# Kernel optimization log

Hardware: AMD Instinct MI355X
Metric: run time of the kernel (lower is better)

The kernel has to match this reference:

```python
import jax, jax.numpy as jnp
import numpy as np

B, ND, NE, D, H = 2, 2048, 2048, 1024, 16
HD = D // H
DFF = 4 * D
EPS = 1e-5


def setup_inputs() -> dict:
    key = jax.random.key(0)
    ks = jax.random.split(key, 16)
    s = lambda fan_in: 1.0 / np.sqrt(fan_in)
    inp = {
        'x': jax.random.normal(ks[0], (B, ND, D), jnp.float32),
        'memory': jax.random.normal(ks[1], (B, NE, D), jnp.float32),
        'ln1_g': jnp.ones((D,), jnp.float32), 'ln1_b': jnp.zeros((D,), jnp.float32),
        'Wqkv': jax.random.normal(ks[2], (D, 3 * D), jnp.float32) * s(D),
        'Wo_sa': jax.random.normal(ks[3], (D, D), jnp.float32) * s(D),
        'bo_sa': jnp.zeros((D,), jnp.float32),
        'ln2_g': jnp.ones((D,), jnp.float32), 'ln2_b': jnp.zeros((D,), jnp.float32),
        'Wq': jax.random.normal(ks[4], (D, D), jnp.float32) * s(D),
        'Wk': jax.random.normal(ks[5], (D, D), jnp.float32) * s(D),
        'Wv': jax.random.normal(ks[6], (D, D), jnp.float32) * s(D),
        'Wo_ca': jax.random.normal(ks[7], (D, D), jnp.float32) * s(D),
        'bo_ca': jnp.zeros((D,), jnp.float32),
        'ln3_g': jnp.ones((D,), jnp.float32), 'ln3_b': jnp.zeros((D,), jnp.float32),
        'W1': jax.random.normal(ks[8], (D, DFF), jnp.float32) * s(D),
        'b1': jnp.zeros((DFF,), jnp.float32),
        'W2': jax.random.normal(ks[9], (DFF, D), jnp.float32) * s(DFF),
        'b2': jnp.zeros((D,), jnp.float32),
        'attn_mask': jnp.tril(jnp.ones((ND, ND), jnp.bool_)),
    }
    return inp


def _layernorm(x, g, b):
    mu = jnp.mean(x, axis=-1, keepdims=True)
    var = jnp.mean(jnp.square(x - mu), axis=-1, keepdims=True)
    return (x - mu) * jax.lax.rsqrt(var + EPS) * g + b


def _heads(t, n):  # (B,N,D) -> (B,H,N,HD)
    Bn = t.shape[0]
    return t.reshape(Bn, n, H, HD).transpose(0, 2, 1, 3)


def _attend(q, k, v, mask=None):
    scale = HD ** -0.5
    scores = jnp.einsum('bhqd,bhkd->bhqk', q, k) * scale
    if mask is not None:
        scores = jnp.where(mask, scores, -jnp.inf)
    attn = jax.nn.softmax(scores, axis=-1)
    out = jnp.einsum('bhqk,bhkd->bhqd', attn, v)
    Bn, _, Nq, _ = out.shape
    return out.transpose(0, 2, 1, 3).reshape(Bn, Nq, D)


def reference(x, memory, ln1_g, ln1_b, Wqkv, Wo_sa, bo_sa, ln2_g, ln2_b,
              Wq, Wk, Wv, Wo_ca, bo_ca, ln3_g, ln3_b, W1, b1, W2, b2, attn_mask):
    # --- masked self-attention ---
    h = _layernorm(x, ln1_g, ln1_b)
    qkv = (h @ Wqkv).reshape(B, ND, 3, H, HD).transpose(2, 0, 3, 1, 4)  # (3,B,H,N,HD)
    q, k, v = qkv[0], qkv[1], qkv[2]
    sa = _attend(q, k, v, attn_mask[None, None]) @ Wo_sa + bo_sa
    x = x + sa
    # --- cross-attention ---
    h = _layernorm(x, ln2_g, ln2_b)
    q = _heads(h @ Wq, ND)
    k = _heads(memory @ Wk, NE)
    v = _heads(memory @ Wv, NE)
    ca = _attend(q, k, v) @ Wo_ca + bo_ca
    x = x + ca
    # --- FFN ---
    h = _layernorm(x, ln3_g, ln3_b)
    x = x + (jax.nn.gelu(h @ W1 + b1, approximate=False) @ W2 + b2)
    return x
```

## Files before the change

kernel.cpp:

```cpp
#include <hip/hip_runtime.h>
#include <hip/hip_bf16.h>
#include <math.h>

#define B_   2
#define ND_  2048
#define NE_  2048
#define D_   1024
#define H_   16
#define HD_  64
#define DFF_ 4096
#define T_   4096

typedef __attribute__((ext_vector_type(8))) short bf16x8;
typedef __attribute__((ext_vector_type(4))) float f32x4;

#if __has_builtin(__builtin_amdgcn_exp2f)
#define EXP2(x) __builtin_amdgcn_exp2f(x)
#else
#define EXP2(x) exp2f(x)
#endif

__device__ __forceinline__ short f2bf(float f) {
  union { float f; unsigned u; } v; v.f = f;
  return (short)((v.u + 0x7FFFu + ((v.u >> 16) & 1u)) >> 16);
}
__device__ __forceinline__ float bf2f(short s) {
  union { unsigned u; float f; } v; v.u = ((unsigned)(unsigned short)s) << 16;
  return v.f;
}

typedef const __attribute__((address_space(1))) void gvoid_t;
typedef __attribute__((address_space(3))) void lvoid_t;

__device__ __forceinline__ void gload16(const void* src, void* dst) {
  __builtin_amdgcn_global_load_lds((gvoid_t*)src, (lvoid_t*)dst, 16, 0, 0);
}

__global__ __launch_bounds__(256) void wt_cast(const float* __restrict__ in,
                                               short* __restrict__ out,
                                               int K, int N) {
  __shared__ float t[32][33];
  const int tx = threadIdx.x, ty = threadIdx.y;
  const int n0 = blockIdx.x * 32, k0 = blockIdx.y * 32;
#pragma unroll
  for (int i = 0; i < 4; ++i)
    t[ty + i * 8][tx] = in[(size_t)(k0 + ty + i * 8) * N + n0 + tx];
  __syncthreads();
#pragma unroll
  for (int i = 0; i < 4; ++i)
    out[(size_t)(n0 + ty + i * 8) * K + k0 + tx] = f2bf(t[tx][ty + i * 8]);
}

__global__ __launch_bounds__(256) void wt_cast5(const float* __restrict__ i0,
                                                const float* __restrict__ i1,
                                                const float* __restrict__ i2,
                                                const float* __restrict__ i3,
                                                const float* __restrict__ i4,
                                                short* __restrict__ o0,
                                                short* __restrict__ o1,
                                                short* __restrict__ o2,
                                                short* __restrict__ o3,
                                                short* __restrict__ o4) {
  const int z = blockIdx.z;
  const float* in = z == 0 ? i0 : z == 1 ? i1 : z == 2 ? i2 : z == 3 ? i3 : i4;
  short* out      = z == 0 ? o0 : z == 1 ? o1 : z == 2 ? o2 : z == 3 ? o3 : o4;
  __shared__ float t[32][33];
  const int tx = threadIdx.x, ty = threadIdx.y;
  const int n0 = blockIdx.x * 32, k0 = blockIdx.y * 32;
#pragma unroll
  for (int i = 0; i < 4; ++i)
    t[ty + i * 8][tx] = in[(size_t)(k0 + ty + i * 8) * 1024 + n0 + tx];
  __syncthreads();
#pragma unroll
  for (int i = 0; i < 4; ++i)
    out[(size_t)(n0 + ty + i * 8) * 1024 + k0 + tx] = f2bf(t[tx][ty + i * 8]);
}

__global__ __launch_bounds__(256) void castf2b(const float* __restrict__ in,
                                               short* __restrict__ out) {
  const int i = blockIdx.x * 256 + threadIdx.x;
  float4 v = ((const float4*)in)[i];
  short4 o;
  o.x = f2bf(v.x); o.y = f2bf(v.y); o.z = f2bf(v.z); o.w = f2bf(v.w);
  ((short4*)out)[i] = o;
}

__global__ __launch_bounds__(256) void ln_kernel(const float* __restrict__ x,
                                                 const float* __restrict__ g,
                                                 const float* __restrict__ b,
                                                 short* __restrict__ out) {
  const int row = blockIdx.x;
  const int tid = threadIdx.x;
  const float* xr = x + (size_t)row * D_;
  float4 v = reinterpret_cast<const float4*>(xr)[tid];
  float s  = v.x + v.y + v.z + v.w;
  float s2 = v.x * v.x + v.y * v.y + v.z * v.z + v.w * v.w;
#pragma unroll
  for (int m = 1; m < 64; m <<= 1) {
    s  += __shfl_xor(s, m);
    s2 += __shfl_xor(s2, m);
  }
  __shared__ float ss[4], ss2[4];
  const int w = tid >> 6;
  if ((tid & 63) == 0) { ss[w] = s; ss2[w] = s2; }
  __syncthreads();
  s  = ss[0] + ss[1] + ss[2] + ss[3];
  s2 = ss2[0] + ss2[1] + ss2[2] + ss2[3];
  const float mu   = s * (1.0f / D_);
  const float var  = s2 * (1.0f / D_) - mu * mu;
  const float rstd = rsqrtf(var + 1e-5f);
  float4 gv = reinterpret_cast<const float4*>(g)[tid];
  float4 bv = reinterpret_cast<const float4*>(b)[tid];
  short4 o;
  o.x = f2bf((v.x - mu) * rstd * gv.x + bv.x);
  o.y = f2bf((v.y - mu) * rstd * gv.y + bv.y);
  o.z = f2bf((v.z - mu) * rstd * gv.z + bv.z);
  o.w = f2bf((v.w - mu) * rstd * gv.w + bv.w);
  reinterpret_cast<short4*>(out + (size_t)row * D_)[tid] = o;
}

__global__ __launch_bounds__(256) void ln_fused(const float* __restrict__ xprev,
                                                const short* delta,
                                                const float* __restrict__ pbias,
                                                const float* __restrict__ g,
                                                const float* __restrict__ b,
                                                short* out_ln,
                                                float* __restrict__ out_x) {
  const int row = blockIdx.x;
  const int tid = threadIdx.x;
  float4 v = reinterpret_cast<const float4*>(xprev + (size_t)row * D_)[tid];
  short4 dv = reinterpret_cast<const short4*>(delta + (size_t)row * D_)[tid];
  float4 pb = reinterpret_cast<const float4*>(pbias)[tid];
  v.x += bf2f(dv.x) + pb.x;
  v.y += bf2f(dv.y) + pb.y;
  v.z += bf2f(dv.z) + pb.z;
  v.w += bf2f(dv.w) + pb.w;
  float s  = v.x + v.y + v.z + v.w;
  float s2 = v.x * v.x + v.y * v.y + v.z * v.z + v.w * v.w;
#pragma unroll
  for (int m = 1; m < 64; m <<= 1) {
    s  += __shfl_xor(s, m);
    s2 += __shfl_xor(s2, m);
  }
  __shared__ float ss[4], ss2[4];
  const int w = tid >> 6;
  if ((tid & 63) == 0) { ss[w] = s; ss2[w] = s2; }
  __syncthreads();
  s  = ss[0] + ss[1] + ss[2] + ss[3];
  s2 = ss2[0] + ss2[1] + ss2[2] + ss2[3];
  const float mu   = s * (1.0f / D_);
  const float var  = s2 * (1.0f / D_) - mu * mu;
  const float rstd = rsqrtf(var + 1e-5f);
  reinterpret_cast<float4*>(out_x + (size_t)row * D_)[tid] = v;
  float4 gv = reinterpret_cast<const float4*>(g)[tid];
  float4 bv = reinterpret_cast<const float4*>(b)[tid];
  short4 o;
  o.x = f2bf((v.x - mu) * rstd * gv.x + bv.x);
  o.y = f2bf((v.y - mu) * rstd * gv.y + bv.y);
  o.z = f2bf((v.z - mu) * rstd * gv.z + bv.z);
  o.w = f2bf((v.w - mu) * rstd * gv.w + bv.w);
  reinterpret_cast<short4*>(out_ln + (size_t)row * D_)[tid] = o;
}

__global__ __launch_bounds__(256) void addbias(const float* __restrict__ x,
                                               const short* __restrict__ delta,
                                               const float* __restrict__ bias,
                                               float* __restrict__ out) {
  const int i = blockIdx.x * 256 + threadIdx.x;
  float4 v = ((const float4*)x)[i];
  short4 dv = ((const short4*)delta)[i];
  const int col = (i * 4) & (D_ - 1);
  float4 pb = *(const float4*)(bias + col);
  v.x += bf2f(dv.x) + pb.x;
  v.y += bf2f(dv.y) + pb.y;
  v.z += bf2f(dv.z) + pb.z;
  v.w += bf2f(dv.w) + pb.w;
  ((float4*)out)[i] = v;
}

template <int MODE>
__global__ __launch_bounds__(256) void gemm_bt(const short* __restrict__ A,
                                               const short* __restrict__ Bt,
                                               const float* __restrict__ bias,
                                               void* __restrict__ Cout,
                                               int M, int N, int K) {
  __shared__ short As[128 * 32];
  __shared__ short Bs[128 * 32];
  const int tid = threadIdx.x;
  const int gx = gridDim.x;
  const int nwg = gx * gridDim.y;
  int lin = blockIdx.y * gx + blockIdx.x;
  lin = (lin & 7) * (nwg >> 3) + (lin >> 3);
  const int m0 = (lin / gx) * 128, n0 = (lin % gx) * 128;
  const int wave = tid >> 6, lane = tid & 63;
  const int wm = (wave >> 1) * 64, wn = (wave & 1) * 64;
  const int lr = lane & 15, lg = lane >> 4;

  f32x4 acc[4][4];
#pragma unroll
  for (int i = 0; i < 4; ++i)
#pragma unroll
    for (int j = 0; j < 4; ++j) acc[i][j] = f32x4{0.f, 0.f, 0.f, 0.f};

  const int e0 = tid * 8, e1 = 2048 + tid * 8;
  const int r0 = e0 >> 5, c0 = e0 & 31;
  const int r1 = e1 >> 5, c1 = e1 & 31;
  const size_t ar0 = (size_t)(m0 + r0) * K, ar1 = (size_t)(m0 + r1) * K;
  const size_t br0 = (size_t)(n0 + r0) * K, br1 = (size_t)(n0 + r1) * K;

  for (int k0 = 0; k0 < K; k0 += 32) {
    gload16(A + ar0 + k0 + c0, As + e0);
    gload16(A + ar1 + k0 + c1, As + e1);
    gload16(Bt + br0 + k0 + c0, Bs + e0);
    gload16(Bt + br1 + k0 + c1, Bs + e1);
    __syncthreads();
    bf16x8 af[4], bfr[4];
#pragma unroll
    for (int mi = 0; mi < 4; ++mi)
      af[mi] = *(const bf16x8*)(As + (wm + mi * 16 + lr) * 32 + lg * 8);
#pragma unroll
    for (int ni = 0; ni < 4; ++ni)
      bfr[ni] = *(const bf16x8*)(Bs + (wn + ni * 16 + lr) * 32 + lg * 8);
#pragma unroll
    for (int mi = 0; mi < 4; ++mi)
#pragma unroll
      for (int ni = 0; ni < 4; ++ni)
        acc[mi][ni] = __builtin_amdgcn_mfma_f32_16x16x32_bf16(
            af[mi], bfr[ni], acc[mi][ni], 0, 0, 0);
    __syncthreads();
  }

#pragma unroll
  for (int mi = 0; mi < 4; ++mi) {
    const int row = m0 + wm + mi * 16 + lg * 4;
#pragma unroll
    for (int ni = 0; ni < 4; ++ni) {
      const int col = n0 + wn + ni * 16 + lr;
#pragma unroll
      for (int r = 0; r < 4; ++r) {
        const size_t idx = (size_t)(row + r) * N + col;
        const float v = acc[mi][ni][r];
        if (MODE == 0) {
          ((short*)Cout)[idx] = f2bf(v);
        } else {
          const float tt = v + bias[col];
          const float yy = fmaf(tt * tt * tt, 0.044715f, tt);
          const float e = EXP2(yy * -2.3022343813918633f);
          ((short*)Cout)[idx] = f2bf(tt / (1.0f + e));
        }
      }
    }
  }
}

__global__ __launch_bounds__(256) void gemm_bt3(const short* __restrict__ A0,
                                                const short* __restrict__ A1,
                                                const short* __restrict__ A2,
                                                const short* __restrict__ B0,
                                                const short* __restrict__ B1,
                                                const short* __restrict__ B2,
                                                short* __restrict__ C0,
                                                short* __restrict__ C1,
                                                short* __restrict__ C2,
                                                int M, int N, int K) {
  const int z = blockIdx.z;
  const short* A  = z == 0 ? A0 : (z == 1 ? A1 : A2);
  const short* Bt = z == 0 ? B0 : (z == 1 ? B1 : B2);
  short* C        = z == 0 ? C0 : (z == 1 ? C1 : C2);

  __shared__ short As[128 * 32];
  __shared__ short Bs[128 * 32];
  const int tid = threadIdx.x;
  const int gx = gridDim.x;
  const int nwg = gx * gridDim.y;
  int lin = blockIdx.y * gx + blockIdx.x;
  lin = (lin & 7) * (nwg >> 3) + (lin >> 3);
  const int m0 = (lin / gx) * 128, n0 = (lin % gx) * 128;
  const int wave = tid >> 6, lane = tid & 63;
  const int wm = (wave >> 1) * 64, wn = (wave & 1) * 64;
  const int lr = lane & 15, lg = lane >> 4;

  f32x4 acc[4][4];
#pragma unroll
  for (int i = 0; i < 4; ++i)
#pragma unroll
    for (int j = 0; j < 4; ++j) acc[i][j] = f32x4{0.f, 0.f, 0.f, 0.f};

  const int e0 = tid * 8, e1 = 2048 + tid * 8;
  const int r0 = e0 >> 5, c0 = e0 & 31;
  const int r1 = e1 >> 5, c1 = e1 & 31;
  const size_t ar0 = (size_t)(m0 + r0) * K, ar1 = (size_t)(m0 + r1) * K;
  const size_t br0 = (size_t)(n0 + r0) * K, br1 = (size_t)(n0 + r1) * K;

  for (int k0 = 0; k0 < K; k0 += 32) {
    gload16(A + ar0 + k0 + c0, As + e0);
    gload16(A + ar1 + k0 + c1, As + e1);
    gload16(Bt + br0 + k0 + c0, Bs + e0);
    gload16(Bt + br1 + k0 + c1, Bs + e1);
    __syncthreads();
    bf16x8 af[4], bfr[4];
#pragma unroll
    for (int mi = 0; mi < 4; ++mi)
      af[mi] = *(const bf16x8*)(As + (wm + mi * 16 + lr) * 32 + lg * 8);
#pragma unroll
    for (int ni = 0; ni < 4; ++ni)
      bfr[ni] = *(const bf16x8*)(Bs + (wn + ni * 16 + lr) * 32 + lg * 8);
#pragma unroll
    for (int mi = 0; mi < 4; ++mi)
#pragma unroll
      for (int ni = 0; ni < 4; ++ni)
        acc[mi][ni] = __builtin_amdgcn_mfma_f32_16x16x32_bf16(
            af[mi], bfr[ni], acc[mi][ni], 0, 0, 0);
    __syncthreads();
  }

#pragma unroll
  for (int mi = 0; mi < 4; ++mi) {
    const int row = m0 + wm + mi * 16 + lg * 4;
#pragma unroll
    for (int ni = 0; ni < 4; ++ni) {
      const int col = n0 + wn + ni * 16 + lr;
#pragma unroll
      for (int r = 0; r < 4; ++r)
        C[(size_t)(row + r) * N + col] = f2bf(acc[mi][ni][r]);
    }
  }
}

__global__ __launch_bounds__(256) void gemm_bt64(const short* __restrict__ A,
                                                 const short* __restrict__ Bt,
                                                 short* __restrict__ Cout,
                                                 int M, int N, int K) {
  __shared__ short As[2][64 * 32];
  __shared__ short Bs[2][128 * 32];
  const int tid = threadIdx.x;
  const int gx = gridDim.x;
  const int nwg = gx * gridDim.y;
  int lin = blockIdx.y * gx + blockIdx.x;
  lin = (lin & 7) * (nwg >> 3) + (lin >> 3);
  const int m0 = (lin / gx) * 64, n0 = (lin % gx) * 128;
  const int wave = tid >> 6, lane = tid & 63;
  const int wn = wave * 32;
  const int lr = lane & 15, lg = lane >> 4;

  f32x4 acc[4][2];
#pragma unroll
  for (int i = 0; i < 4; ++i)
#pragma unroll
    for (int j = 0; j < 2; ++j) acc[i][j] = f32x4{0.f, 0.f, 0.f, 0.f};

  const int ea = tid * 8;
  const int ra = ea >> 5, ca = ea & 31;
  const int e0 = tid * 8, e1 = 2048 + tid * 8;
  const int r0 = e0 >> 5, c0 = e0 & 31;
  const int r1 = e1 >> 5, c1 = e1 & 31;
  const size_t ar = (size_t)(m0 + ra) * K;
  const size_t br0 = (size_t)(n0 + r0) * K, br1 = (size_t)(n0 + r1) * K;

  auto stage = [&](int buf, int k0) {
    gload16(A + ar + k0 + ca, &As[buf][0] + ea);
    gload16(Bt + br0 + k0 + c0, &Bs[buf][0] + e0);
    gload16(Bt + br1 + k0 + c1, &Bs[buf][0] + e1);
  };

  stage(0, 0);
  __syncthreads();
  int cur = 0;
  for (int k0 = 0; k0 < K; k0 += 32) {
    if (k0 + 32 < K) stage(cur ^ 1, k0 + 32);
    const short* Ab = &As[cur][0];
    const short* Bb = &Bs[cur][0];
    bf16x8 af[4], bfr[2];
#pragma unroll
    for (int mi = 0; mi < 4; ++mi)
      af[mi] = *(const bf16x8*)(Ab + (mi * 16 + lr) * 32 + lg * 8);
#pragma unroll
    for (int ni = 0; ni < 2; ++ni)
      bfr[ni] = *(const bf16x8*)(Bb + (wn + ni * 16 + lr) * 32 + lg * 8);
#pragma unroll
    for (int mi = 0; mi < 4; ++mi)
#pragma unroll
      for (int ni = 0; ni < 2; ++ni)
        acc[mi][ni] = __builtin_amdgcn_mfma_f32_16x16x32_bf16(
            af[mi], bfr[ni], acc[mi][ni], 0, 0, 0);
    __syncthreads();
    cur ^= 1;
  }

#pragma unroll
  for (int mi = 0; mi < 4; ++mi) {
    const int row = m0 + mi * 16 + lg * 4;
#pragma unroll
    for (int ni = 0; ni < 2; ++ni) {
      const int col = n0 + wn + ni * 16 + lr;
#pragma unroll
      for (int r = 0; r < 4; ++r)
        Cout[(size_t)(row + r) * N + col] = f2bf(acc[mi][ni][r]);
    }
  }
}

__global__ __launch_bounds__(256) void vtrans(const short* __restrict__ in,
                                              short* __restrict__ out,
                                              int ldi, int N) {
  const int bh = blockIdx.z;
  const int b = bh >> 4, h = bh & 15;
  const short* ib = in + (size_t)b * N * ldi + h * HD_;
  short* ob = out + (size_t)bh * HD_ * N;
  __shared__ short t[32][33];
  const int tx = threadIdx.x, ty = threadIdx.y;
  const int n0 = blockIdx.x * 32, d0 = blockIdx.y * 32;
#pragma unroll
  for (int i = 0; i < 4; ++i)
    t[ty + i * 8][tx] = ib[(size_t)(n0 + ty + i * 8) * ldi + d0 + tx];
  __syncthreads();
#pragma unroll
  for (int i = 0; i < 4; ++i)
    ob[(size_t)(d0 + ty + i * 8) * N + n0 + tx] = t[tx][ty + i * 8];
}

__global__ __launch_bounds__(256) void flash(const short* __restrict__ Q,
                                             const short* __restrict__ Kp,
                                             const short* __restrict__ Vt,
                                             short* __restrict__ O,
                                             int ldq, int ldk, int ldo,
                                             int NK, int causal) {
  const int bh = blockIdx.x;
  int qb = blockIdx.y;
  if (causal) qb = (qb < 16) ? (2 * qb) : (63 - 2 * qb);
  const int b = bh >> 4, h = bh & 15;
  const int q0 = qb * 64;
  const int tid = threadIdx.x, wave = tid >> 6, lane = tid & 63;
  const int lr = lane & 15, lg = lane >> 4;
  const int lx = lr & 7;

  const short* Qb = Q + (size_t)b * ND_ * ldq + h * HD_;
  const short* Kb = Kp + (size_t)b * NK * ldk + h * HD_;
  const short* Vb = Vt + (size_t)bh * HD_ * NK;
  short* Ob = O + (size_t)b * ND_ * ldo + h * HD_;

  __shared__ short Ks[2][64 * 64];
  __shared__ short Vs[2][64 * 64];
  __shared__ short Ps[4][16 * 64];

  const int qrow = q0 + wave * 16 + lr;
  const bf16x8 qf0 = *(const bf16x8*)(Qb + (size_t)qrow * ldq + lg * 8);
  const bf16x8 qf1 = *(const bf16x8*)(Qb + (size_t)qrow * ldq + 32 + lg * 8);

  const bf16x8 ONES = {0x3F80, 0x3F80, 0x3F80, 0x3F80,
                       0x3F80, 0x3F80, 0x3F80, 0x3F80};

  f32x4 oacc[4];
  f32x4 lacc = f32x4{0.f, 0.f, 0.f, 0.f};
  float m_own = -1e30f;
#pragma unroll
  for (int i = 0; i < 4; ++i) oacc[i] = f32x4{0.f, 0.f, 0.f, 0.f};

  const int sr0 = tid >> 3;
  const int ssw = ((tid & 7) ^ (sr0 & 7)) * 8;
  const int e0 = tid * 8, e1 = 2048 + tid * 8;

  const float SC = 0.18033688011112042f;

  short* Pw = &Ps[wave][0];
  const int pbase = lr * 64 + (lg & 1) * 4;

  auto stage = [&](int buf, int k0) {
    gload16(Kb + (size_t)(k0 + sr0) * ldk + ssw, &Ks[buf][0] + e0);
    gload16(Kb + (size_t)(k0 + 32 + sr0) * ldk + ssw, &Ks[buf][0] + e1);
    gload16(Vb + (size_t)sr0 * NK + k0 + ssw, &Vs[buf][0] + e0);
    gload16(Vb + (size_t)(32 + sr0) * NK + k0 + ssw, &Vs[buf][0] + e1);
  };

  const int nkt = causal ? (qb + 1) : (NK / 64);
  stage(0, 0);
  __syncthreads();
  int cur = 0;
  for (int t = 0; t < nkt; ++t) {
    const int k0 = t * 64;
    if (t + 1 < nkt) stage(cur ^ 1, k0 + 64);
    const short* Ksb = &Ks[cur][0];
    const short* Vsb = &Vs[cur][0];

    f32x4 st[4];
#pragma unroll
    for (int kb = 0; kb < 4; ++kb) {
      const bf16x8 kf0 = *(const bf16x8*)(Ksb + (kb * 16 + lr) * 64 + ((lg ^ lx) * 8));
      const bf16x8 kf1 = *(const bf16x8*)(Ksb + (kb * 16 + lr) * 64 + (((4 + lg) ^ lx) * 8));
      st[kb] = f32x4{0.f, 0.f, 0.f, 0.f};
      st[kb] = __builtin_amdgcn_mfma_f32_16x16x32_bf16(kf0, qf0, st[kb], 0, 0, 0);
      st[kb] = __builtin_amdgcn_mfma_f32_16x16x32_bf16(kf1, qf1, st[kb], 0, 0, 0);
    }
    if (causal && t == nkt - 1) {
#pragma unroll
      for (int kb = 0; kb < 4; ++kb)
#pragma unroll
        for (int r = 0; r < 4; ++r)
          if ((k0 + kb * 16 + lg * 4 + r) > qrow) st[kb][r] = -3.0e38f;
    }

    float rm = st[0][0];
#pragma unroll
    for (int kb = 0; kb < 4; ++kb)
#pragma unroll
      for (int r = 0; r < 4; ++r)
        if (kb || r) rm = fmaxf(rm, st[kb][r]);
    rm = fmaxf(rm, __shfl_xor(rm, 16));
    rm = fmaxf(rm, __shfl_xor(rm, 32));

    if (!__all(rm - m_own <= 44.f)) {
      const float nm = fmaxf(m_own, rm);
      const float fac = EXP2((m_own - nm) * SC);
      m_own = nm;
      const float fr0 = __shfl(fac, (lg << 2) + 0);
      const float fr1 = __shfl(fac, (lg << 2) + 1);
      const float fr2 = __shfl(fac, (lg << 2) + 2);
      const float fr3 = __shfl(fac, (lg << 2) + 3);
#pragma unroll
      for (int db = 0; db < 4; ++db) {
        oacc[db][0] *= fr0; oacc[db][1] *= fr1;
        oacc[db][2] *= fr2; oacc[db][3] *= fr3;
      }
      lacc[0] *= fr0; lacc[1] *= fr1; lacc[2] *= fr2; lacc[3] *= fr3;
    }
    const float nmsc = m_own * SC;
#pragma unroll
    for (int kb = 0; kb < 4; ++kb)
#pragma unroll
      for (int r = 0; r < 4; ++r)
        st[kb][r] = EXP2(fmaf(st[kb][r], SC, -nmsc));

#pragma unroll
    for (int kb = 0; kb < 4; ++kb) {
      union { unsigned u[2]; unsigned long long ull; } pk;
      asm("v_cvt_pk_bf16_f32 %0, %1, %2"
          : "=v"(pk.u[0]) : "v"(st[kb][0]), "v"(st[kb][1]));
      asm("v_cvt_pk_bf16_f32 %0, %1, %2"
          : "=v"(pk.u[1]) : "v"(st[kb][2]), "v"(st[kb][3]));
      const int cs = kb * 2 + (lg >> 1);
      *(unsigned long long*)(Pw + pbase + ((cs ^ lx) * 8)) = pk.ull;
    }
    const bf16x8 pf0 = *(const bf16x8*)(Pw + lr * 64 + ((lg ^ lx) * 8));
    const bf16x8 pf1 = *(const bf16x8*)(Pw + lr * 64 + (((4 + lg) ^ lx) * 8));

#pragma unroll
    for (int db = 0; db < 4; ++db) {
      const bf16x8 vf0 = *(const bf16x8*)(Vsb + (db * 16 + lr) * 64 + ((lg ^ lx) * 8));
      const bf16x8 vf1 = *(const bf16x8*)(Vsb + (db * 16 + lr) * 64 + (((4 + lg) ^ lx) * 8));
      oacc[db] = __builtin_amdgcn_mfma_f32_16x16x32_bf16(pf0, vf0, oacc[db], 0, 0, 0);
      oacc[db] = __builtin_amdgcn_mfma_f32_16x16x32_bf16(pf1, vf1, oacc[db], 0, 0, 0);
    }
    lacc = __builtin_amdgcn_mfma_f32_16x16x32_bf16(pf0, ONES, lacc, 0, 0, 0);
    lacc = __builtin_amdgcn_mfma_f32_16x16x32_bf16(pf1, ONES, lacc, 0, 0, 0);
    __syncthreads();
    cur ^= 1;
  }
#pragma unroll
  for (int db = 0; db < 4; ++db)
#pragma unroll
    for (int r = 0; r < 4; ++r) {
      const int q = q0 + wave * 16 + lg * 4 + r;
      Ob[(size_t)q * ldo + db * 16 + lr] = f2bf(oacc[db][r] / lacc[r]);
    }
}

extern "C" void kernel_launch(void* const* d_in, const int* in_sizes, int n_in,
                              void* d_out, int out_size, void* d_ws, size_t ws_size,
                              hipStream_t stream) {
  const float* x      = (const float*)d_in[0];
  const float* memory = (const float*)d_in[1];
  const float* ln1_g  = (const float*)d_in[2];
  const float* ln1_b  = (const float*)d_in[3];
  const float* Wqkv   = (const float*)d_in[4];
  const float* Wo_sa  = (const float*)d_in[5];
  const float* bo_sa  = (const float*)d_in[6];
  const float* ln2_g  = (const float*)d_in[7];
  const float* ln2_b  = (const float*)d_in[8];
  const float* Wq     = (const float*)d_in[9];
  const float* Wk     = (const float*)d_in[10];
  const float* Wv     = (const float*)d_in[11];
  const float* Wo_ca  = (const float*)d_in[12];
  const float* bo_ca  = (const float*)d_in[13];
  const float* ln3_g  = (const float*)d_in[14];
  const float* ln3_b  = (const float*)d_in[15];
  const float* W1     = (const float*)d_in[16];
  const float* b1     = (const float*)d_in[17];
  const float* W2     = (const float*)d_in[18];
  const float* b2     = (const float*)d_in[19];

  char* ws = (char*)d_ws;
  size_t o = 0;
  auto alloc = [&](size_t bytes) { char* p = ws + o; o += bytes; return p; };
  short* wqkv_t = (short*)alloc((size_t)3072 * 1024 * 2);
  short* wosa_t = (short*)alloc((size_t)1024 * 1024 * 2);
  short* wq_t   = (short*)alloc((size_t)1024 * 1024 * 2);
  short* wk_t   = (short*)alloc((size_t)1024 * 1024 * 2);
  short* wv_t   = (short*)alloc((size_t)1024 * 1024 * 2);
  short* woca_t = (short*)alloc((size_t)1024 * 1024 * 2);
  short* w1_t   = (short*)alloc((size_t)4096 * 1024 * 2);
  short* w2_t   = (short*)alloc((size_t)1024 * 4096 * 2);
  short* hbf    = (short*)alloc((size_t)T_ * 1024 * 2);
  short* bufa   = (short*)alloc((size_t)T_ * 3072 * 2);
  short* vt     = (short*)alloc((size_t)32 * 64 * 2048 * 2);
  short* attn   = (short*)alloc((size_t)T_ * 1024 * 2);
  short* membf  = (short*)alloc((size_t)T_ * 1024 * 2);
  float* x1     = (float*)alloc((size_t)T_ * 1024 * 4);
  float* x2     = (float*)alloc((size_t)T_ * 1024 * 4);
  if (o > ws_size) return;

  short* ffn = bufa;
  short* qca = bufa;
  short* kca = bufa + (size_t)T_ * 1024;
  short* vca = bufa + (size_t)2 * T_ * 1024;

  const dim3 tb(32, 8);

  wt_cast<<<dim3(3072 / 32, 1024 / 32), tb, 0, stream>>>(Wqkv, wqkv_t, 1024, 3072);
  wt_cast5<<<dim3(32, 32, 5), tb, 0, stream>>>(Wo_sa, Wq, Wk, Wv, Wo_ca,
                                               wosa_t, wq_t, wk_t, wv_t, woca_t);
  wt_cast<<<dim3(4096 / 32, 1024 / 32), tb, 0, stream>>>(W1, w1_t, 1024, 4096);
  wt_cast<<<dim3(1024 / 32, 4096 / 32), tb, 0, stream>>>(W2, w2_t, 4096, 1024);
  castf2b<<<dim3((T_ * 1024) / (256 * 4)), 256, 0, stream>>>(memory, membf);

  ln_kernel<<<dim3(T_), 256, 0, stream>>>(x, ln1_g, ln1_b, hbf);
  gemm_bt<0><<<dim3(3072 / 128, T_ / 128), 256, 0, stream>>>(
      hbf, wqkv_t, nullptr, bufa, T_, 3072, 1024);
  vtrans<<<dim3(ND_ / 32, HD_ / 32, 32), tb, 0, stream>>>(bufa + 2048, vt, 3072, ND_);
  flash<<<dim3(32, ND_ / 64), 256, 0, stream>>>(
      bufa, bufa + 1024, vt, attn, 3072, 3072, 1024, ND_, 1);
  gemm_bt64<<<dim3(1024 / 128, T_ / 64), 256, 0, stream>>>(
      attn, wosa_t, hbf, T_, 1024, 1024);
  ln_fused<<<dim3(T_), 256, 0, stream>>>(x, hbf, bo_sa, ln2_g, ln2_b, hbf, x1);

  gemm_bt3<<<dim3(1024 / 128, T_ / 128, 3), 256, 0, stream>>>(
      hbf, membf, membf, wq_t, wk_t, wv_t, qca, kca, vca, T_, 1024, 1024);
  vtrans<<<dim3(NE_ / 32, HD_ / 32, 32), tb, 0, stream>>>(vca, vt, 1024, NE_);
  flash<<<dim3(32, ND_ / 64), 256, 0, stream>>>(
      qca, kca, vt, attn, 1024, 1024, 1024, NE_, 0);
  gemm_bt64<<<dim3(1024 / 128, T_ / 64), 256, 0, stream>>>(
      attn, woca_t, hbf, T_, 1024, 1024);
  ln_fused<<<dim3(T_), 256, 0, stream>>>(x1, hbf, bo_ca, ln3_g, ln3_b, hbf, x2);

  gemm_bt<2><<<dim3(4096 / 128, T_ / 128), 256, 0, stream>>>(
      hbf, w1_t, b1, ffn, T_, 4096, 1024);
  gemm_bt64<<<dim3(1024 / 128, T_ / 64), 256, 0, stream>>>(
      ffn, w2_t, hbf, T_, 1024, 4096);
  addbias<<<dim3((T_ * 1024) / (256 * 4)), 256, 0, stream>>>(
      x2, hbf, b2, (float*)d_out);
}
```

Measured before the change: 411.6 us.

## Double-buffer GEMM smem tiles and use 128-query flash blocks with 8 waves

Measured after the change: 387.9 us. 5.8% less time.

```diff
diff --git a/kernel.cpp b/kernel.cpp
--- a/kernel.cpp
+++ b/kernel.cpp
@@ -184,8 +184,8 @@
                                                const float* __restrict__ bias,
                                                void* __restrict__ Cout,
                                                int M, int N, int K) {
-  __shared__ short As[128 * 32];
-  __shared__ short Bs[128 * 32];
+  __shared__ short As[2][128 * 32];
+  __shared__ short Bs[2][128 * 32];
   const int tid = threadIdx.x;
   const int gx = gridDim.x;
   const int nwg = gx * gridDim.y;
@@ -208,19 +208,27 @@
   const size_t ar0 = (size_t)(m0 + r0) * K, ar1 = (size_t)(m0 + r1) * K;
   const size_t br0 = (size_t)(n0 + r0) * K, br1 = (size_t)(n0 + r1) * K;
 
+  auto stage = [&](int buf, int k0) {
+    gload16(A + ar0 + k0 + c0, &As[buf][0] + e0);
+    gload16(A + ar1 + k0 + c1, &As[buf][0] + e1);
+    gload16(Bt + br0 + k0 + c0, &Bs[buf][0] + e0);
+    gload16(Bt + br1 + k0 + c1, &Bs[buf][0] + e1);
+  };
+
+  stage(0, 0);
+  __syncthreads();
+  int cur = 0;
   for (int k0 = 0; k0 < K; k0 += 32) {
-    gload16(A + ar0 + k0 + c0, As + e0);
-    gload16(A + ar1 + k0 + c1, As + e1);
-    gload16(Bt + br0 + k0 + c0, Bs + e0);
-    gload16(Bt + br1 + k0 + c1, Bs + e1);
-    __syncthreads();
+    if (k0 + 32 < K) stage(cur ^ 1, k0 + 32);
+    const short* Ab = &As[cur][0];
+    const short* Bb = &Bs[cur][0];
     bf16x8 af[4], bfr[4];
 #pragma unroll
     for (int mi = 0; mi < 4; ++mi)
-      af[mi] = *(const bf16x8*)(As + (wm + mi * 16 + lr) * 32 + lg * 8);
+      af[mi] = *(const bf16x8*)(Ab + (wm + mi * 16 + lr) * 32 + lg * 8);
 #pragma unroll
     for (int ni = 0; ni < 4; ++ni)
-      bfr[ni] = *(const bf16x8*)(Bs + (wn + ni * 16 + lr) * 32 + lg * 8);
+      bfr[ni] = *(const bf16x8*)(Bb + (wn + ni * 16 + lr) * 32 + lg * 8);
 #pragma unroll
     for (int mi = 0; mi < 4; ++mi)
 #pragma unroll
@@ -228,6 +236,7 @@
         acc[mi][ni] = __builtin_amdgcn_mfma_f32_16x16x32_bf16(
             af[mi], bfr[ni], acc[mi][ni], 0, 0, 0);
     __syncthreads();
+    cur ^= 1;
   }
 
 #pragma unroll
@@ -268,8 +277,8 @@
   const short* Bt = z == 0 ? B0 : (z == 1 ? B1 : B2);
   short* C        = z == 0 ? C0 : (z == 1 ? C1 : C2);
 
-  __shared__ short As[128 * 32];
-  __shared__ short Bs[128 * 32];
+  __shared__ short As[2][128 * 32];
+  __shared__ short Bs[2][128 * 32];
   const int tid = threadIdx.x;
   const int gx = gridDim.x;
   const int nwg = gx * gridDim.y;
@@ -292,19 +301,27 @@
   const size_t ar0 = (size_t)(m0 + r0) * K, ar1 = (size_t)(m0 + r1) * K;
   const size_t br0 = (size_t)(n0 + r0) * K, br1 = (size_t)(n0 + r1) * K;
 
+  auto stage = [&](int buf, int k0) {
+    gload16(A + ar0 + k0 + c0, &As[buf][0] + e0);
+    gload16(A + ar1 + k0 + c1, &As[buf][0] + e1);
+    gload16(Bt + br0 + k0 + c0, &Bs[buf][0] + e0);
+    gload16(Bt + br1 + k0 + c1, &Bs[buf][0] + e1);
+  };
+
+  stage(0, 0);
+  __syncthreads();
+  int cur = 0;
   for (int k0 = 0; k0 < K; k0 += 32) {
-    gload16(A + ar0 + k0 + c0, As + e0);
-    gload16(A + ar1 + k0 + c1, As + e1);
-    gload16(Bt + br0 + k0 + c0, Bs + e0);
-    gload16(Bt + br1 + k0 + c1, Bs + e1);
-    __syncthreads();
+    if (k0 + 32 < K) stage(cur ^ 1, k0 + 32);
+    const short* Ab = &As[cur][0];
+    const short* Bb = &Bs[cur][0];
     bf16x8 af[4], bfr[4];
 #pragma unroll
     for (int mi = 0; mi < 4; ++mi)
-      af[mi] = *(const bf16x8*)(As + (wm + mi * 16 + lr) * 32 + lg * 8);
+      af[mi] = *(const bf16x8*)(Ab + (wm + mi * 16 + lr) * 32 + lg * 8);
 #pragma unroll
     for (int ni = 0; ni < 4; ++ni)
-      bfr[ni] = *(const bf16x8*)(Bs + (wn + ni * 16 + lr) * 32 + lg * 8);
+      bfr[ni] = *(const bf16x8*)(Bb + (wn + ni * 16 + lr) * 32 + lg * 8);
 #pragma unroll
     for (int mi = 0; mi < 4; ++mi)
 #pragma unroll
@@ -312,6 +329,7 @@
         acc[mi][ni] = __builtin_amdgcn_mfma_f32_16x16x32_bf16(
             af[mi], bfr[ni], acc[mi][ni], 0, 0, 0);
     __syncthreads();
+    cur ^= 1;
   }
 
 #pragma unroll
@@ -419,7 +437,7 @@
     ob[(size_t)(d0 + ty + i * 8) * N + n0 + tx] = t[tx][ty + i * 8];
 }
 
-__global__ __launch_bounds__(256) void flash(const short* __restrict__ Q,
+__global__ __launch_bounds__(512) void flash(const short* __restrict__ Q,
                                              const short* __restrict__ Kp,
                                              const short* __restrict__ Vt,
                                              short* __restrict__ O,
@@ -427,9 +445,9 @@
                                              int NK, int causal) {
   const int bh = blockIdx.x;
   int qb = blockIdx.y;
-  if (causal) qb = (qb < 16) ? (2 * qb) : (63 - 2 * qb);
+  if (causal) qb = (qb < 8) ? (2 * qb) : (31 - 2 * qb);
   const int b = bh >> 4, h = bh & 15;
-  const int q0 = qb * 64;
+  const int q0 = qb * 128;
   const int tid = threadIdx.x, wave = tid >> 6, lane = tid & 63;
   const int lr = lane & 15, lg = lane >> 4;
   const int lx = lr & 7;
@@ -441,7 +459,7 @@
 
   __shared__ short Ks[2][64 * 64];
   __shared__ short Vs[2][64 * 64];
-  __shared__ short Ps[4][16 * 64];
+  __shared__ short Ps[8][16 * 64];
 
   const int qrow = q0 + wave * 16 + lr;
   const bf16x8 qf0 = *(const bf16x8*)(Qb + (size_t)qrow * ldq + lg * 8);
@@ -458,7 +476,7 @@
 
   const int sr0 = tid >> 3;
   const int ssw = ((tid & 7) ^ (sr0 & 7)) * 8;
-  const int e0 = tid * 8, e1 = 2048 + tid * 8;
+  const int e0 = tid * 8;
 
   const float SC = 0.18033688011112042f;
 
@@ -467,91 +485,91 @@
 
   auto stage = [&](int buf, int k0) {
     gload16(Kb + (size_t)(k0 + sr0) * ldk + ssw, &Ks[buf][0] + e0);
-    gload16(Kb + (size_t)(k0 + 32 + sr0) * ldk + ssw, &Ks[buf][0] + e1);
     gload16(Vb + (size_t)sr0 * NK + k0 + ssw, &Vs[buf][0] + e0);
-    gload16(Vb + (size_t)(32 + sr0) * NK + k0 + ssw, &Vs[buf][0] + e1);
   };
 
-  const int nkt = causal ? (qb + 1) : (NK / 64);
+  const int nkt = causal ? (2 * qb + 2) : (NK / 64);
   stage(0, 0);
   __syncthreads();
   int cur = 0;
   for (int t = 0; t < nkt; ++t) {
     const int k0 = t * 64;
     if (t + 1 < nkt) stage(cur ^ 1, k0 + 64);
-    const short* Ksb = &Ks[cur][0];
-    const short* Vsb = &Vs[cur][0];
-
-    f32x4 st[4];
-#pragma unroll
-    for (int kb = 0; kb < 4; ++kb) {
-      const bf16x8 kf0 = *(const bf16x8*)(Ksb + (kb * 16 + lr) * 64 + ((lg ^ lx) * 8));
-      const bf16x8 kf1 = *(const bf16x8*)(Ksb + (kb * 16 + lr) * 64 + (((4 + lg) ^ lx) * 8));
-      st[kb] = f32x4{0.f, 0.f, 0.f, 0.f};
-      st[kb] = __builtin_amdgcn_mfma_f32_16x16x32_bf16(kf0, qf0, st[kb], 0, 0, 0);
-      st[kb] = __builtin_amdgcn_mfma_f32_16x16x32_bf16(kf1, qf1, st[kb], 0, 0, 0);
+    if (!causal || k0 <= q0 + wave * 16 + 15) {
+      const short* Ksb = &Ks[cur][0];
+      const short* Vsb = &Vs[cur][0];
+
+      f32x4 st[4];
+#pragma unroll
+      for (int kb = 0; kb < 4; ++kb) {
+        const bf16x8 kf0 = *(const bf16x8*)(Ksb + (kb * 16 + lr) * 64 + ((lg ^ lx) * 8));
+        const bf16x8 kf1 = *(const bf16x8*)(Ksb + (kb * 16 + lr) * 64 + (((4 + lg) ^ lx) * 8));
+        st[kb] = f32x4{0.f, 0.f, 0.f, 0.f};
+        st[kb] = __builtin_amdgcn_mfma_f32_16x16x32_bf16(kf0, qf0, st[kb], 0, 0, 0);
+        st[kb] = __builtin_amdgcn_mfma_f32_16x16x32_bf16(kf1, qf1, st[kb], 0, 0, 0);
+      }
+      if (causal && k0 + 63 > q0 + wave * 16) {
+#pragma unroll
+        for (int kb = 0; kb < 4; ++kb)
+#pragma unroll
+          for (int r = 0; r < 4; ++r)
+            if ((k0 + kb * 16 + lg * 4 + r) > qrow) st[kb][r] = -3.0e38f;
+      }
+
+      float rm = st[0][0];
+#pragma unroll
+      for (int kb = 0; kb < 4; ++kb)
+#pragma unroll
+        for (int r = 0; r < 4; ++r)
+          if (kb || r) rm = fmaxf(rm, st[kb][r]);
+      rm = fmaxf(rm, __shfl_xor(rm, 16));
+      rm = fmaxf(rm, __shfl_xor(rm, 32));
+
+      if (!__all(rm - m_own <= 44.f)) {
+        const float nm = fmaxf(m_own, rm);
+        const float fac = EXP2((m_own - nm) * SC);
+        m_own = nm;
+        const float fr0 = __shfl(fac, (lg << 2) + 0);
+        const float fr1 = __shfl(fac, (lg << 2) + 1);
+        const float fr2 = __shfl(fac, (lg << 2) + 2);
+        const float fr3 = __shfl(fac, (lg << 2) + 3);
+#pragma unroll
+        for (int db = 0; db < 4; ++db) {
+          oacc[db][0] *= fr0; oacc[db][1] *= fr1;
+          oacc[db][2] *= fr2; oacc[db][3] *= fr3;
+        }
+        lacc[0] *= fr0; lacc[1] *= fr1; lacc[2] *= fr2; lacc[3] *= fr3;
+      }
+      const float nmsc = m_own * SC;
+#pragma unroll
+      for (int kb = 0; kb < 4; ++kb)
+#pragma unroll
+        for (int r = 0; r < 4; ++r)
+          st[kb][r] = EXP2(fmaf(st[kb][r], SC, -nmsc));
+
+#pragma unroll
+      for (int kb = 0; kb < 4; ++kb) {
+        union { unsigned u[2]; unsigned long long ull; } pk;
+        asm("v_cvt_pk_bf16_f32 %0, %1, %2"
+            : "=v"(pk.u[0]) : "v"(st[kb][0]), "v"(st[kb][1]));
+        asm("v_cvt_pk_bf16_f32 %0, %1, %2"
+            : "=v"(pk.u[1]) : "v"(st[kb][2]), "v"(st[kb][3]));
+        const int cs = kb * 2 + (lg >> 1);
+        *(unsigned long long*)(Pw + pbase + ((cs ^ lx) * 8)) = pk.ull;
+      }
+      const bf16x8 pf0 = *(const bf16x8*)(Pw + lr * 64 + ((lg ^ lx) * 8));
+      const bf16x8 pf1 = *(const bf16x8*)(Pw + lr * 64 + (((4 + lg) ^ lx) * 8));
+
+#pragma unroll
+      for (int db = 0; db < 4; ++db) {
+        const bf16x8 vf0 = *(const bf16x8*)(Vsb + (db * 16 + lr) * 64 + ((lg ^ lx) * 8));
+        const bf16x8 vf1 = *(const bf16x8*)(Vsb + (db * 16 + lr) * 64 + (((4 + lg) ^ lx) * 8));
+        oacc[db] = __builtin_amdgcn_mfma_f32_16x16x32_bf16(pf0, vf0, oacc[db], 0, 0, 0);
+        oacc[db] = __builtin_amdgcn_mfma_f32_16x16x32_bf16(pf1, vf1, oacc[db], 0, 0, 0);
+      }
+      lacc = __builtin_amdgcn_mfma_f32_16x16x32_bf16(pf0, ONES, lacc, 0, 0, 0);
+      lacc = __builtin_amdgcn_mfma_f32_16x16x32_bf16(pf1, ONES, lacc, 0, 0, 0);
     }
-    if (causal && t == nkt - 1) {
-#pragma unroll
-      for (int kb = 0; kb < 4; ++kb)
-#pragma unroll
-        for (int r = 0; r < 4; ++r)
-          if ((k0 + kb * 16 + lg * 4 + r) > qrow) st[kb][r] = -3.0e38f;
-    }
-
-    float rm = st[0][0];
-#pragma unroll
-    for (int kb = 0; kb < 4; ++kb)
-#pragma unroll
-      for (int r = 0; r < 4; ++r)
-        if (kb || r) rm = fmaxf(rm, st[kb][r]);
-    rm = fmaxf(rm, __shfl_xor(rm, 16));
-    rm = fmaxf(rm, __shfl_xor(rm, 32));
-
-    if (!__all(rm - m_own <= 44.f)) {
-      const float nm = fmaxf(m_own, rm);
-      const float fac = EXP2((m_own - nm) * SC);
-      m_own = nm;
-      const float fr0 = __shfl(fac, (lg << 2) + 0);
-      const float fr1 = __shfl(fac, (lg << 2) + 1);
-      const float fr2 = __shfl(fac, (lg << 2) + 2);
-      const float fr3 = __shfl(fac, (lg << 2) + 3);
-#pragma unroll
-      for (int db = 0; db < 4; ++db) {
-        oacc[db][0] *= fr0; oacc[db][1] *= fr1;
-        oacc[db][2] *= fr2; oacc[db][3] *= fr3;
-      }
-      lacc[0] *= fr0; lacc[1] *= fr1; lacc[2] *= fr2; lacc[3] *= fr3;
-    }
-    const float nmsc = m_own * SC;
-#pragma unroll
-    for (int kb = 0; kb < 4; ++kb)
-#pragma unroll
-      for (int r = 0; r < 4; ++r)
-        st[kb][r] = EXP2(fmaf(st[kb][r], SC, -nmsc));
-
-#pragma unroll
-    for (int kb = 0; kb < 4; ++kb) {
-      union { unsigned u[2]; unsigned long long ull; } pk;
-      asm("v_cvt_pk_bf16_f32 %0, %1, %2"
-          : "=v"(pk.u[0]) : "v"(st[kb][0]), "v"(st[kb][1]));
-      asm("v_cvt_pk_bf16_f32 %0, %1, %2"
-          : "=v"(pk.u[1]) : "v"(st[kb][2]), "v"(st[kb][3]));
-      const int cs = kb * 2 + (lg >> 1);
-      *(unsigned long long*)(Pw + pbase + ((cs ^ lx) * 8)) = pk.ull;
-    }
-    const bf16x8 pf0 = *(const bf16x8*)(Pw + lr * 64 + ((lg ^ lx) * 8));
-    const bf16x8 pf1 = *(const bf16x8*)(Pw + lr * 64 + (((4 + lg) ^ lx) * 8));
-
-#pragma unroll
-    for (int db = 0; db < 4; ++db) {
-      const bf16x8 vf0 = *(const bf16x8*)(Vsb + (db * 16 + lr) * 64 + ((lg ^ lx) * 8));
-      const bf16x8 vf1 = *(const bf16x8*)(Vsb + (db * 16 + lr) * 64 + (((4 + lg) ^ lx) * 8));
-      oacc[db] = __builtin_amdgcn_mfma_f32_16x16x32_bf16(pf0, vf0, oacc[db], 0, 0, 0);
-      oacc[db] = __builtin_amdgcn_mfma_f32_16x16x32_bf16(pf1, vf1, oacc[db], 0, 0, 0);
-    }
-    lacc = __builtin_amdgcn_mfma_f32_16x16x32_bf16(pf0, ONES, lacc, 0, 0, 0);
-    lacc = __builtin_amdgcn_mfma_f32_16x16x32_bf16(pf1, ONES, lacc, 0, 0, 0);
     __syncthreads();
     cur ^= 1;
   }
@@ -626,7 +644,7 @@
   gemm_bt<0><<<dim3(3072 / 128, T_ / 128), 256, 0, stream>>>(
       hbf, wqkv_t, nullptr, bufa, T_, 3072, 1024);
   vtrans<<<dim3(ND_ / 32, HD_ / 32, 32), tb, 0, stream>>>(bufa + 2048, vt, 3072, ND_);
-  flash<<<dim3(32, ND_ / 64), 256, 0, stream>>>(
+  flash<<<dim3(32, ND_ / 128), 512, 0, stream>>>(
       bufa, bufa + 1024, vt, attn, 3072, 3072, 1024, ND_, 1);
   gemm_bt64<<<dim3(1024 / 128, T_ / 64), 256, 0, stream>>>(
       attn, wosa_t, hbf, T_, 1024, 1024);
@@ -635,7 +653,7 @@
   gemm_bt3<<<dim3(1024 / 128, T_ / 128, 3), 256, 0, stream>>>(
       hbf, membf, membf, wq_t, wk_t, wv_t, qca, kca, vca, T_, 1024, 1024);
   vtrans<<<dim3(NE_ / 32, HD_ / 32, 32), tb, 0, stream>>>(vca, vt, 1024, NE_);
-  flash<<<dim3(32, ND_ / 64), 256, 0, stream>>>(
+  flash<<<dim3(32, ND_ / 128), 512, 0, stream>>>(
       qca, kca, vt, attn, 1024, 1024, 1024, NE_, 0);
   gemm_bt64<<<dim3(1024 / 128, T_ / 64), 256, 0, stream>>>(
       attn, woca_t, hbf, T_, 1024, 1024);
```
